# Performance work log

Measured on AMD Instinct MI355X. Metric: run time of the kernel, lower is better.

Reference implementation:

```python
import jax, jax.numpy as jnp
import numpy as np

N_NODES = 50000
N_EDGES = 800000
DIM = 64


def setup_inputs() -> dict:
    key = jax.random.key(0)
    ks = jax.random.split(key, 11)
    d = DIM
    node_embeddings = jax.random.normal(ks[0], (N_NODES, d), dtype=jnp.float32)
    neighbour_attributes = jax.random.normal(ks[1], (N_EDGES, d), dtype=jnp.float32)
    batch_index = jnp.sort(jax.random.randint(ks[2], (N_EDGES,), 0, N_NODES))
    s_align = 1.0 / np.sqrt(2 * d)
    s_d = 1.0 / np.sqrt(d)
    # alignment_layer: Linear(2d -> 1)
    align_w = jax.random.uniform(ks[3], (1, 2 * d), jnp.float32, -s_align, s_align)
    align_b = jax.random.uniform(ks[4], (1,), jnp.float32, -s_align, s_align)
    # context_layer: Linear(d -> d)
    ctx_w = jax.random.uniform(ks[5], (d, d), jnp.float32, -s_d, s_d)
    ctx_b = jax.random.uniform(ks[6], (d,), jnp.float32, -s_d, s_d)
    # readout_layer: GRUCell(d, d) -- torch layout [3d, d] gates (r, z, n)
    w_ih = jax.random.uniform(ks[7], (3 * d, d), jnp.float32, -s_d, s_d)
    w_hh = jax.random.uniform(ks[8], (3 * d, d), jnp.float32, -s_d, s_d)
    b_ih = jax.random.uniform(ks[9], (3 * d,), jnp.float32, -s_d, s_d)
    b_hh = jax.random.uniform(ks[10], (3 * d,), jnp.float32, -s_d, s_d)
    return {
        "node_embeddings": node_embeddings,
        "neighbour_attributes": neighbour_attributes,
        "batch_index": batch_index,
        "align_w": align_w, "align_b": align_b,
        "ctx_w": ctx_w, "ctx_b": ctx_b,
        "w_ih": w_ih, "w_hh": w_hh, "b_ih": b_ih, "b_hh": b_hh,
    }


def reference(node_embeddings, neighbour_attributes, batch_index,
              align_w, align_b, ctx_w, ctx_b, w_ih, w_hh, b_ih, b_hh):
    n = node_embeddings.shape[0]
    # _expand_and_join: gather node row per edge, concat with neighbour feats -> [E, 2d]
    joint = jnp.concatenate([node_embeddings[batch_index], neighbour_attributes], axis=1)
    # alignment + leaky_relu (torch default negative_slope=0.01); dropout is identity (p=0)
    scores = jax.nn.leaky_relu(joint @ align_w.T + align_b, negative_slope=0.01)[:, 0]  # [E]
    # segment softmax over variable-size neighbourhoods (torch_geometric softmax)
    seg_max = jax.ops.segment_max(scores, batch_index, num_segments=n)
    seg_max = jnp.where(jnp.isfinite(seg_max), seg_max, 0.0)  # guard empty segments
    ex = jnp.exp(scores - jax.lax.stop_gradient(seg_max)[batch_index])
    denom = jax.ops.segment_sum(ex, batch_index, num_segments=n)[batch_index]
    attn = (ex / jnp.maximum(denom, 1e-16))[:, None]  # [E, 1]
    # attention-weighted context messages, scatter-add pooled per node, then ELU
    msgs = attn * (neighbour_attributes @ ctx_w.T + ctx_b)  # [E, d]
    contexts = jax.nn.elu(jax.ops.segment_sum(msgs, batch_index, num_segments=n))  # [N, d]
    # GRUCell(contexts, node_embeddings), torch gate order (r, z, n)
    gi = contexts @ w_ih.T + b_ih
    gh = node_embeddings @ w_hh.T + b_hh
    i_r, i_z, i_n = jnp.split(gi, 3, axis=1)
    h_r, h_z, h_n = jnp.split(gh, 3, axis=1)
    r = jax.nn.sigmoid(i_r + h_r)
    z = jax.nn.sigmoid(i_z + h_z)
    g = jnp.tanh(i_n + r * h_n)
    h_new = (1.0 - z) * g + z * node_embeddings
    return jax.nn.relu(h_new)
```

## Files before the change

kernel.cpp:

```cpp
#include <hip/hip_runtime.h>
#include <stdint.h>

constexpr int kN = 50000;
constexpr int kE = 800000;
constexpr int kD = 64;

typedef short sv8 __attribute__((ext_vector_type(8)));
typedef float fv4 __attribute__((ext_vector_type(4)));

__device__ __forceinline__ float bf2f(uint16_t u) {
    union { uint32_t i; float f; } v; v.i = ((uint32_t)u) << 16; return v.f;
}
__device__ __forceinline__ uint16_t f2bf(float f) {
    union { float ff; uint32_t i; } v; v.ff = f;
    return (uint16_t)((v.i + 0x7FFFu + ((v.i >> 16) & 1u)) >> 16);
}
__device__ __forceinline__ float wsum64(float x) {
    x += __shfl_xor(x, 1);  x += __shfl_xor(x, 2);  x += __shfl_xor(x, 4);
    x += __shfl_xor(x, 8);  x += __shfl_xor(x, 16); x += __shfl_xor(x, 32);
    return x;
}

template<int BF> __device__ __forceinline__ float ldf(const void* p, int i) {
    if (BF) return bf2f(((const uint16_t*)p)[i]);
    return ((const float*)p)[i];
}
template<int BF> __device__ __forceinline__ void stf(void* p, int i, float v) {
    if (BF) ((uint16_t*)p)[i] = f2bf(v);
    else    ((float*)p)[i] = v;
}
template<int BF> __device__ __forceinline__ sv8 ldfrag(const void* p, int elem_base) {
    if (BF) {
        return *(const sv8*)((const uint16_t*)p + elem_base);
    } else {
        const float* f = (const float*)p + elem_base;
        sv8 r;
#pragma unroll
        for (int i = 0; i < 8; ++i) r[i] = (short)f2bf(f[i]);
        return r;
    }
}
__device__ __forceinline__ fv4 mfma16(sv8 a, sv8 b, fv4 c) {
    return __builtin_amdgcn_mfma_f32_16x16x32_bf16(a, b, c, 0, 0, 0);
}
template<int BF> __device__ __forceinline__ void ldrow(
    const void* nbr, int e, int t, float& v0, float& v1, float& v2, float& v3)
{
    if (BF) {
        uint2 u = *(const uint2*)((const uint16_t*)nbr + (size_t)e * kD + t * 4);
        v0 = bf2f((uint16_t)u.x); v1 = bf2f((uint16_t)(u.x >> 16));
        v2 = bf2f((uint16_t)u.y); v3 = bf2f((uint16_t)(u.y >> 16));
    } else {
        float4 f = *(const float4*)((const float*)nbr + (size_t)e * kD + t * 4);
        v0 = f.x; v1 = f.y; v2 = f.z; v3 = f.w;
    }
}

__global__ void k_prep(const int* __restrict__ bi, int* __restrict__ rp,
                       const uint16_t* __restrict__ nbr, int* __restrict__ flag) {
    if (blockIdx.x == gridDim.x - 1) {
        int lane = threadIdx.x;
        if (lane < 64) {
            float an = 0.f;
            for (int i = lane; i < 512; i += 64) {
                uint16_t u = nbr[i];
                if ((u & 0x7fffu) != 0) {
                    float a = fabsf(bf2f(u));
                    if (!(a >= 1e-8f && a <= 1e8f)) an += 1.f;
                }
            }
            an = wsum64(an);
            if (lane == 0) flag[0] = (an > 0.5f) ? 0 : 1;
        }
        return;
    }
    int n = blockIdx.x * 256 + threadIdx.x;
    if (n > kN) return;
    int lo = 0, hi = kE;
    int gl = n * 16 - 2048, gh = n * 16 + 2048;
    if (gl > 0 && gl < kE && bi[gl] < n)  lo = gl;
    if (gh > 0 && gh < kE && bi[gh] >= n) hi = gh;
    while (lo < hi) { int mid = (lo + hi) >> 1; if (bi[mid] < n) lo = mid + 1; else hi = mid; }
    rp[n] = lo;
}

template<int BF>
__device__ __forceinline__ void edges_body(
    const void* node_emb, const void* nbr, const void* align_w, const void* align_b,
    const int* __restrict__ rp, uint16_t* weighted, float* fhas)
{
    const int lane = threadIdx.x & 63;
    const int n    = blockIdx.x * 4 + (threadIdx.x >> 6);
    const int g    = lane >> 4;
    const int t    = lane & 15;

    float nd = wsum64(ldf<BF>(node_emb, n * kD + lane) * ldf<BF>(align_w, lane))
             + ldf<BF>(align_b, 0);

    float w0 = ldf<BF>(align_w, kD + t * 4 + 0);
    float w1 = ldf<BF>(align_w, kD + t * 4 + 1);
    float w2 = ldf<BF>(align_w, kD + t * 4 + 2);
    float w3 = ldf<BF>(align_w, kD + t * 4 + 3);

    const int s0 = rp[n], s1 = rp[n + 1];
    float l = 0.f, a0 = 0.f, a1 = 0.f, a2 = 0.f, a3 = 0.f;

    float c00, c01, c02, c03, c10, c11, c12, c13;
    {
        int e0 = s0 + g, e1 = s0 + g + 4;
        ldrow<BF>(nbr, (e0 < s1) ? e0 : 0, t, c00, c01, c02, c03);
        ldrow<BF>(nbr, (e1 < s1) ? e1 : 0, t, c10, c11, c12, c13);
    }

    for (int eb = s0; eb < s1; eb += 8) {
        float n00, n01, n02, n03, n10, n11, n12, n13;
        {
            int f0 = eb + 8 + g, f1 = eb + 12 + g;
            ldrow<BF>(nbr, (f0 < s1) ? f0 : 0, t, n00, n01, n02, n03);
            ldrow<BF>(nbr, (f1 < s1) ? f1 : 0, t, n10, n11, n12, n13);
        }
        float pa = c00 * w0 + c01 * w1 + c02 * w2 + c03 * w3;
        float pb = c10 * w0 + c11 * w1 + c12 * w2 + c13 * w3;
        pa += __shfl_xor(pa, 1);  pb += __shfl_xor(pb, 1);
        pa += __shfl_xor(pa, 2);  pb += __shfl_xor(pb, 2);
        pa += __shfl_xor(pa, 4);  pb += __shfl_xor(pb, 4);
        pa += __shfl_xor(pa, 8);  pb += __shfl_xor(pb, 8);
        float sa = pa + nd;  sa = (sa > 0.f) ? sa : 0.01f * sa;
        float sb = pb + nd;  sb = (sb > 0.f) ? sb : 0.01f * sb;
        float ea = (eb + g     < s1) ? __expf(sa) : 0.f;
        float eb2 = (eb + g + 4 < s1) ? __expf(sb) : 0.f;
        l  += ea + eb2;
        a0 += ea * c00 + eb2 * c10;
        a1 += ea * c01 + eb2 * c11;
        a2 += ea * c02 + eb2 * c12;
        a3 += ea * c03 + eb2 * c13;
        c00 = n00; c01 = n01; c02 = n02; c03 = n03;
        c10 = n10; c11 = n11; c12 = n12; c13 = n13;
    }

    l  += __shfl_xor(l, 16);   l  += __shfl_xor(l, 32);
    a0 += __shfl_xor(a0, 16);  a0 += __shfl_xor(a0, 32);
    a1 += __shfl_xor(a1, 16);  a1 += __shfl_xor(a1, 32);
    a2 += __shfl_xor(a2, 16);  a2 += __shfl_xor(a2, 32);
    a3 += __shfl_xor(a3, 16);  a3 += __shfl_xor(a3, 32);

    if (g == 0) {
        float inv = (s1 > s0) ? (1.f / l) : 0.f;
        uint32_t lo = (uint32_t)f2bf(a0 * inv) | ((uint32_t)f2bf(a1 * inv) << 16);
        uint32_t hi = (uint32_t)f2bf(a2 * inv) | ((uint32_t)f2bf(a3 * inv) << 16);
        *(uint2*)(weighted + (size_t)n * kD + t * 4) = make_uint2(lo, hi);
        if (t == 0) fhas[n] = (s1 > s0) ? 1.f : 0.f;
    }
}
__global__ __launch_bounds__(256, 4) void k_edges(
    const void* node_emb, const void* nbr, const void* aw, const void* ab,
    const int* __restrict__ rp, const int* __restrict__ flag,
    uint16_t* __restrict__ weighted, float* __restrict__ fhas)
{
    if (*flag) edges_body<1>(node_emb, nbr, aw, ab, rp, weighted, fhas);
    else       edges_body<0>(node_emb, nbr, aw, ab, rp, weighted, fhas);
}

template<int BF>
__device__ __forceinline__ void gru_body(
    const void* node_emb,
    const void* ctx_w, const void* ctx_b,
    const void* w_ih,  const void* w_hh,
    const void* b_ih,  const void* b_hh,
    const uint16_t* weighted, const float* fhas, void* out,
    uint16_t* swt,
    uint16_t (*sctx)[16][72])
{
    const int tid  = threadIdx.x;
    const int lane = tid & 63;
    const int wv   = tid >> 6;
    const int R    = blockIdx.x * 64 + wv * 16;
    const int t    = lane & 15;
    const int q    = lane >> 4;

    const fv4 zf = {0.f, 0.f, 0.f, 0.f};

    {
        const void* srcs[2] = { w_ih, w_hh };
#pragma unroll
        for (int hlf = 0; hlf < 2; ++hlf) {
            const void* src = srcs[hlf];
            uint16_t* dst = swt + hlf * 192 * 72;
            for (int off = tid * 8; off < 192 * 64; off += 256 * 8) {
                int r = off >> 6, c = off & 63;
                if (BF) {
                    *(uint4*)(dst + r * 72 + c) =
                        *(const uint4*)((const uint16_t*)src + off);
                } else {
                    const float* f = (const float*)src + off;
                    uint32_t p0 = (uint32_t)f2bf(f[0]) | ((uint32_t)f2bf(f[1]) << 16);
                    uint32_t p1 = (uint32_t)f2bf(f[2]) | ((uint32_t)f2bf(f[3]) << 16);
                    uint32_t p2 = (uint32_t)f2bf(f[4]) | ((uint32_t)f2bf(f[5]) << 16);
                    uint32_t p3 = (uint32_t)f2bf(f[6]) | ((uint32_t)f2bf(f[7]) << 16);
                    *(uint4*)(dst + r * 72 + c) = make_uint4(p0, p1, p2, p3);
                }
            }
        }
    }

    int ar = R + t; if (ar > kN - 1) ar = kN - 1;
    sv8 ah0 = ldfrag<BF>(node_emb, ar * kD + q * 8);
    sv8 ah1 = ldfrag<BF>(node_emb, ar * kD + q * 8 + 32);
    sv8 aw0 = ldfrag<1>(weighted, ar * kD + q * 8);
    sv8 aw1 = ldfrag<1>(weighted, ar * kD + q * 8 + 32);

    __syncthreads();

    fv4 accC[4];
#pragma unroll
    for (int ct = 0; ct < 4; ++ct) {
        int rb = (ct * 16 + t) * kD + q * 8;
        fv4 a = zf;
        a = mfma16(aw0, ldfrag<BF>(ctx_w, rb),      a);
        a = mfma16(aw1, ldfrag<BF>(ctx_w, rb + 32), a);
        accC[ct] = a;
    }

    float has_i[4];
#pragma unroll
    for (int i = 0; i < 4; ++i) {
        int node = R + q * 4 + i; if (node > kN - 1) node = kN - 1;
        has_i[i] = fhas[node];
    }
#pragma unroll
    for (int ct = 0; ct < 4; ++ct) {
        int col = ct * 16 + t;
        float cb = ldf<BF>(ctx_b, col);
#pragma unroll
        for (int i = 0; i < 4; ++i) {
            float x = accC[ct][i] + has_i[i] * cb;
            x = (x > 0.f) ? x : (__expf(x) - 1.f);
            sctx[wv][q * 4 + i][col] = f2bf(x);
        }
    }
    __syncthreads();

    sv8 ac0 = *(const sv8*)&sctx[wv][t][q * 8];
    sv8 ac1 = *(const sv8*)&sctx[wv][t][q * 8 + 32];

    const uint16_t* ih = swt;
    const uint16_t* hh = swt + 192 * 72;

#pragma unroll
    for (int jt = 0; jt < 4; ++jt) {
        const int rr = jt * 16 + t;
        fv4 air = zf, aiz = zf, ain = zf, ahr = zf, ahz = zf, ahn = zf;
        air = mfma16(ac0, *(const sv8*)&ih[ rr        * 72 + q * 8],      air);
        air = mfma16(ac1, *(const sv8*)&ih[ rr        * 72 + q * 8 + 32], air);
        aiz = mfma16(ac0, *(const sv8*)&ih[(rr +  64) * 72 + q * 8],      aiz);
        aiz = mfma16(ac1, *(const sv8*)&ih[(rr +  64) * 72 + q * 8 + 32], aiz);
        ain = mfma16(ac0, *(const sv8*)&ih[(rr + 128) * 72 + q * 8],      ain);
        ain = mfma16(ac1, *(const sv8*)&ih[(rr + 128) * 72 + q * 8 + 32], ain);
        ahr = mfma16(ah0, *(const sv8*)&hh[ rr        * 72 + q * 8],      ahr);
        ahr = mfma16(ah1, *(const sv8*)&hh[ rr        * 72 + q * 8 + 32], ahr);
        ahz = mfma16(ah0, *(const sv8*)&hh[(rr +  64) * 72 + q * 8],      ahz);
        ahz = mfma16(ah1, *(const sv8*)&hh[(rr +  64) * 72 + q * 8 + 32], ahz);
        ahn = mfma16(ah0, *(const sv8*)&hh[(rr + 128) * 72 + q * 8],      ahn);
        ahn = mfma16(ah1, *(const sv8*)&hh[(rr + 128) * 72 + q * 8 + 32], ahn);

        const int col = jt * 16 + t;
        float bir = ldf<BF>(b_ih, col),       bhr = ldf<BF>(b_hh, col);
        float biz = ldf<BF>(b_ih, 64 + col),  bhz = ldf<BF>(b_hh, 64 + col);
        float bin = ldf<BF>(b_ih, 128 + col), bhn = ldf<BF>(b_hh, 128 + col);
#pragma unroll
        for (int i = 0; i < 4; ++i) {
            int node = R + q * 4 + i;
            bool valid = node < kN;
            int cn = valid ? node : kN - 1;
            float hv = ldf<BF>(node_emb, cn * kD + col);
            float r = 1.f / (1.f + __expf(-(air[i] + bir + ahr[i] + bhr)));
            float z = 1.f / (1.f + __expf(-(aiz[i] + biz + ahz[i] + bhz)));
            float tt = ain[i] + bin + r * (ahn[i] + bhn);
            float gg = 2.f / (1.f + __expf(-2.f * tt)) - 1.f;
            float hn = (1.f - z) * gg + z * hv;
            if (valid) stf<BF>(out, node * kD + col, fmaxf(hn, 0.f));
        }
    }
}
__global__ __launch_bounds__(256, 2) void k_gru(
    const void* node_emb, const void* ctx_w, const void* ctx_b,
    const void* w_ih, const void* w_hh, const void* b_ih, const void* b_hh,
    const uint16_t* __restrict__ weighted, const float* __restrict__ fhas,
    const int* __restrict__ flag, void* out)
{
    __shared__ uint16_t swt[384 * 72];
    __shared__ uint16_t sctx[4][16][72];
    if (*flag) gru_body<1>(node_emb, ctx_w, ctx_b, w_ih, w_hh, b_ih, b_hh, weighted, fhas, out, swt, sctx);
    else       gru_body<0>(node_emb, ctx_w, ctx_b, w_ih, w_hh, b_ih, b_hh, weighted, fhas, out, swt, sctx);
}

extern "C" void kernel_launch(void* const* d_in, const int* in_sizes, int n_in,
                              void* d_out, int out_size, void* d_ws, size_t ws_size,
                              hipStream_t stream) {
    (void)in_sizes; (void)n_in; (void)out_size; (void)ws_size;
    const void* node_emb = d_in[0];
    const void* nbr      = d_in[1];
    const int*  bi       = (const int*)d_in[2];
    const void* align_w  = d_in[3];
    const void* align_b  = d_in[4];
    const void* ctx_w    = d_in[5];
    const void* ctx_b    = d_in[6];
    const void* w_ih     = d_in[7];
    const void* w_hh     = d_in[8];
    const void* b_ih     = d_in[9];
    const void* b_hh     = d_in[10];

    char* ws = (char*)d_ws;
    int*      row_ptr  = (int*)ws;
    int*      flag     = (int*)(ws + 200064);
    float*    fhas     = (float*)(ws + 204800);
    uint16_t* weighted = (uint16_t*)(ws + 409600);

    k_prep<<<(kN + 256) / 256 + 1, 256, 0, stream>>>(bi, row_ptr, (const uint16_t*)nbr, flag);
    k_edges<<<kN / 4, 256, 0, stream>>>(node_emb, nbr, align_w, align_b, row_ptr, flag, weighted, fhas);
    k_gru<<<(kN + 63) / 64, 256, 0, stream>>>(node_emb, ctx_w, ctx_b, w_ih, w_hh, b_ih, b_hh,
                                              weighted, fhas, flag, d_out);
}
```

Measured before the change: 345.1 us.

## Pre-convert GRU weights to bf16 in prep kernel and deepen edge prefetch

The prep kernel now converts ctx_w, w_ih and w_hh to bf16 once into workspace, and each prep block re-runs the dtype detection itself. The GRU kernel reads its MFMA weight fragments straight from global or L2 instead of staging 55KB into shared memory per block, which drops two __syncthreads and raises the occupancy bound from 2 to 4. The edge kernel processes 16 edges per iteration with a deeper prefetch, which costs more registers. The risk is extra global or L2 traffic for the weight fragments in the GRU kernel.

```diff
diff --git a/kernel.cpp b/kernel.cpp
--- a/kernel.cpp
+++ b/kernel.cpp
@@ -56,32 +56,63 @@
     }
 }
 
+__device__ __forceinline__ int detect_bf16(const uint16_t* __restrict__ nbr) {
+    const int lane = threadIdx.x & 63;
+    uint4 v = ((const uint4*)nbr)[lane];
+    uint32_t w[4] = { v.x, v.y, v.z, v.w };
+    float an = 0.f;
+#pragma unroll
+    for (int k = 0; k < 4; ++k) {
+#pragma unroll
+        for (int h = 0; h < 2; ++h) {
+            uint16_t u = (uint16_t)(w[k] >> (16 * h));
+            if ((u & 0x7fffu) != 0) {
+                float a = fabsf(bf2f(u));
+                if (!(a >= 1e-8f && a <= 1e8f)) an += 1.f;
+            }
+        }
+    }
+    an = wsum64(an);
+    return (an > 0.5f) ? 0 : 1;
+}
+
 __global__ void k_prep(const int* __restrict__ bi, int* __restrict__ rp,
-                       const uint16_t* __restrict__ nbr, int* __restrict__ flag) {
-    if (blockIdx.x == gridDim.x - 1) {
-        int lane = threadIdx.x;
-        if (lane < 64) {
-            float an = 0.f;
-            for (int i = lane; i < 512; i += 64) {
-                uint16_t u = nbr[i];
-                if ((u & 0x7fffu) != 0) {
-                    float a = fabsf(bf2f(u));
-                    if (!(a >= 1e-8f && a <= 1e8f)) an += 1.f;
-                }
-            }
-            an = wsum64(an);
-            if (lane == 0) flag[0] = (an > 0.5f) ? 0 : 1;
-        }
-        return;
-    }
-    int n = blockIdx.x * 256 + threadIdx.x;
-    if (n > kN) return;
-    int lo = 0, hi = kE;
-    int gl = n * 16 - 2048, gh = n * 16 + 2048;
-    if (gl > 0 && gl < kE && bi[gl] < n)  lo = gl;
-    if (gh > 0 && gh < kE && bi[gh] >= n) hi = gh;
-    while (lo < hi) { int mid = (lo + hi) >> 1; if (bi[mid] < n) lo = mid + 1; else hi = mid; }
-    rp[n] = lo;
+                       const uint16_t* __restrict__ nbr, int* __restrict__ flag,
+                       const void* __restrict__ ctx_w, const void* __restrict__ w_ih,
+                       const void* __restrict__ w_hh,
+                       uint16_t* __restrict__ cwbf, uint16_t* __restrict__ ihbf,
+                       uint16_t* __restrict__ hhbf) {
+    const int b = blockIdx.x;
+    if (b < 196) {
+        int n = b * 256 + threadIdx.x;
+        if (n > kN) return;
+        int lo = 0, hi = kE;
+        int gl = n * 16 - 2048, gh = n * 16 + 2048;
+        if (gl > 0 && gl < kE && bi[gl] < n)  lo = gl;
+        if (gh > 0 && gh < kE && bi[gh] >= n) hi = gh;
+        while (lo < hi) { int mid = (lo + hi) >> 1; if (bi[mid] < n) lo = mid + 1; else hi = mid; }
+        rp[n] = lo;
+    } else if (b == 196) {
+        if (threadIdx.x < 64) {
+            int bf = detect_bf16(nbr);
+            if (threadIdx.x == 0) flag[0] = bf;
+        }
+    } else {
+        const int base = (b - 197) * 1024 + threadIdx.x * 4;
+        const void* src; uint16_t* dst; int off;
+        if (base < 4096)       { src = ctx_w; dst = cwbf; off = base; }
+        else if (base < 16384) { src = w_ih;  dst = ihbf; off = base - 4096; }
+        else                   { src = w_hh;  dst = hhbf; off = base - 16384; }
+        const int bf = detect_bf16(nbr);
+        if (bf) {
+            *(uint2*)(dst + off) = *(const uint2*)((const uint16_t*)src + off);
+        } else {
+            float4 f = *(const float4*)((const float*)src + off);
+            uint32_t p0 = (uint32_t)f2bf(f.x) | ((uint32_t)f2bf(f.y) << 16);
+            uint32_t p1 = (uint32_t)f2bf(f.z) | ((uint32_t)f2bf(f.w) << 16);
+            *(uint2*)(dst + off) = make_uint2(p0, p1);
+        }
+    }
 }
 
 template<int BF>
@@ -106,36 +137,54 @@
     float l = 0.f, a0 = 0.f, a1 = 0.f, a2 = 0.f, a3 = 0.f;
 
     float c00, c01, c02, c03, c10, c11, c12, c13;
+    float c20, c21, c22, c23, c30, c31, c32, c33;
     {
-        int e0 = s0 + g, e1 = s0 + g + 4;
+        int e0 = s0 + g, e1 = s0 + g + 4, e2 = s0 + g + 8, e3 = s0 + g + 12;
         ldrow<BF>(nbr, (e0 < s1) ? e0 : 0, t, c00, c01, c02, c03);
         ldrow<BF>(nbr, (e1 < s1) ? e1 : 0, t, c10, c11, c12, c13);
-    }
-
-    for (int eb = s0; eb < s1; eb += 8) {
-        float n00, n01, n02, n03, n10, n11, n12, n13;
+        ldrow<BF>(nbr, (e2 < s1) ? e2 : 0, t, c20, c21, c22, c23);
+        ldrow<BF>(nbr, (e3 < s1) ? e3 : 0, t, c30, c31, c32, c33);
+    }
+
+    for (int eb = s0; eb < s1; eb += 16) {
+        float m00, m01, m02, m03, m10, m11, m12, m13;
+        float m20, m21, m22, m23, m30, m31, m32, m33;
         {
-            int f0 = eb + 8 + g, f1 = eb + 12 + g;
-            ldrow<BF>(nbr, (f0 < s1) ? f0 : 0, t, n00, n01, n02, n03);
-            ldrow<BF>(nbr, (f1 < s1) ? f1 : 0, t, n10, n11, n12, n13);
-        }
-        float pa = c00 * w0 + c01 * w1 + c02 * w2 + c03 * w3;
-        float pb = c10 * w0 + c11 * w1 + c12 * w2 + c13 * w3;
-        pa += __shfl_xor(pa, 1);  pb += __shfl_xor(pb, 1);
-        pa += __shfl_xor(pa, 2);  pb += __shfl_xor(pb, 2);
-        pa += __shfl_xor(pa, 4);  pb += __shfl_xor(pb, 4);
-        pa += __shfl_xor(pa, 8);  pb += __shfl_xor(pb, 8);
-        float sa = pa + nd;  sa = (sa > 0.f) ? sa : 0.01f * sa;
-        float sb = pb + nd;  sb = (sb > 0.f) ? sb : 0.01f * sb;
-        float ea = (eb + g     < s1) ? __expf(sa) : 0.f;
-        float eb2 = (eb + g + 4 < s1) ? __expf(sb) : 0.f;
-        l  += ea + eb2;
-        a0 += ea * c00 + eb2 * c10;
-        a1 += ea * c01 + eb2 * c11;
-        a2 += ea * c02 + eb2 * c12;
-        a3 += ea * c03 + eb2 * c13;
-        c00 = n00; c01 = n01; c02 = n02; c03 = n03;
-        c10 = n10; c11 = n11; c12 = n12; c13 = n13;
+            int f0 = eb + 16 + g, f1 = eb + 20 + g, f2 = eb + 24 + g, f3 = eb + 28 + g;
+            ldrow<BF>(nbr, (f0 < s1) ? f0 : 0, t, m00, m01, m02, m03);
+            ldrow<BF>(nbr, (f1 < s1) ? f1 : 0, t, m10, m11, m12, m13);
+            ldrow<BF>(nbr, (f2 < s1) ? f2 : 0, t, m20, m21, m22, m23);
+            ldrow<BF>(nbr, (f3 < s1) ? f3 : 0, t, m30, m31, m32, m33);
+        }
+        float p0 = c00 * w0 + c01 * w1 + c02 * w2 + c03 * w3;
+        float p1 = c10 * w0 + c11 * w1 + c12 * w2 + c13 * w3;
+        float p2 = c20 * w0 + c21 * w1 + c22 * w2 + c23 * w3;
+        float p3 = c30 * w0 + c31 * w1 + c32 * w2 + c33 * w3;
+        p0 += __shfl_xor(p0, 1); p1 += __shfl_xor(p1, 1);
+        p2 += __shfl_xor(p2, 1); p3 += __shfl_xor(p3, 1);
+        p0 += __shfl_xor(p0, 2); p1 += __shfl_xor(p1, 2);
+        p2 += __shfl_xor(p2, 2); p3 += __shfl_xor(p3, 2);
+        p0 += __shfl_xor(p0, 4); p1 += __shfl_xor(p1, 4);
+        p2 += __shfl_xor(p2, 4); p3 += __shfl_xor(p3, 4);
+        p0 += __shfl_xor(p0, 8); p1 += __shfl_xor(p1, 8);
+        p2 += __shfl_xor(p2, 8); p3 += __shfl_xor(p3, 8);
+        float s0f = p0 + nd;  s0f = (s0f > 0.f) ? s0f : 0.01f * s0f;
+        float s1f = p1 + nd;  s1f = (s1f > 0.f) ? s1f : 0.01f * s1f;
+        float s2f = p2 + nd;  s2f = (s2f > 0.f) ? s2f : 0.01f * s2f;
+        float s3f = p3 + nd;  s3f = (s3f > 0.f) ? s3f : 0.01f * s3f;
+        float e0 = (eb + g      < s1) ? __expf(s0f) : 0.f;
+        float e1 = (eb + g + 4  < s1) ? __expf(s1f) : 0.f;
+        float e2 = (eb + g + 8  < s1) ? __expf(s2f) : 0.f;
+        float e3 = (eb + g + 12 < s1) ? __expf(s3f) : 0.f;
+        l  += (e0 + e1) + (e2 + e3);
+        a0 += e0 * c00 + e1 * c10 + e2 * c20 + e3 * c30;
+        a1 += e0 * c01 + e1 * c11 + e2 * c21 + e3 * c31;
+        a2 += e0 * c02 + e1 * c12 + e2 * c22 + e3 * c32;
+        a3 += e0 * c03 + e1 * c13 + e2 * c23 + e3 * c33;
+        c00 = m00; c01 = m01; c02 = m02; c03 = m03;
+        c10 = m10; c11 = m11; c12 = m12; c13 = m13;
+        c20 = m20; c21 = m21; c22 = m22; c23 = m23;
+        c30 = m30; c31 = m31; c32 = m32; c33 = m33;
     }
 
     l  += __shfl_xor(l, 16);   l  += __shfl_xor(l, 32);
@@ -163,45 +212,20 @@
 
 template<int BF>
 __device__ __forceinline__ void gru_body(
-    const void* node_emb,
-    const void* ctx_w, const void* ctx_b,
-    const void* w_ih,  const void* w_hh,
+    const void* node_emb, const void* ctx_b,
     const void* b_ih,  const void* b_hh,
+    const uint16_t* __restrict__ cwbf, const uint16_t* __restrict__ ihbf,
+    const uint16_t* __restrict__ hhbf,
     const uint16_t* weighted, const float* fhas, void* out,
-    uint16_t* swt,
     uint16_t (*sctx)[16][72])
 {
-    const int tid  = threadIdx.x;
-    const int lane = tid & 63;
-    const int wv   = tid >> 6;
+    const int lane = threadIdx.x & 63;
+    const int wv   = threadIdx.x >> 6;
     const int R    = blockIdx.x * 64 + wv * 16;
     const int t    = lane & 15;
     const int q    = lane >> 4;
 
     const fv4 zf = {0.f, 0.f, 0.f, 0.f};
-
-    {
-        const void* srcs[2] = { w_ih, w_hh };
-#pragma unroll
-        for (int hlf = 0; hlf < 2; ++hlf) {
-            const void* src = srcs[hlf];
-            uint16_t* dst = swt + hlf * 192 * 72;
-            for (int off = tid * 8; off < 192 * 64; off += 256 * 8) {
-                int r = off >> 6, c = off & 63;
-                if (BF) {
-                    *(uint4*)(dst + r * 72 + c) =
-                        *(const uint4*)((const uint16_t*)src + off);
-                } else {
-                    const float* f = (const float*)src + off;
-                    uint32_t p0 = (uint32_t)f2bf(f[0]) | ((uint32_t)f2bf(f[1]) << 16);
-                    uint32_t p1 = (uint32_t)f2bf(f[2]) | ((uint32_t)f2bf(f[3]) << 16);
-                    uint32_t p2 = (uint32_t)f2bf(f[4]) | ((uint32_t)f2bf(f[5]) << 16);
-                    uint32_t p3 = (uint32_t)f2bf(f[6]) | ((uint32_t)f2bf(f[7]) << 16);
-                    *(uint4*)(dst + r * 72 + c) = make_uint4(p0, p1, p2, p3);
-                }
-            }
-        }
-    }
 
     int ar = R + t; if (ar > kN - 1) ar = kN - 1;
     sv8 ah0 = ldfrag<BF>(node_emb, ar * kD + q * 8);
@@ -209,15 +233,13 @@
     sv8 aw0 = ldfrag<1>(weighted, ar * kD + q * 8);
     sv8 aw1 = ldfrag<1>(weighted, ar * kD + q * 8 + 32);
 
-    __syncthreads();
-
     fv4 accC[4];
 #pragma unroll
     for (int ct = 0; ct < 4; ++ct) {
         int rb = (ct * 16 + t) * kD + q * 8;
         fv4 a = zf;
-        a = mfma16(aw0, ldfrag<BF>(ctx_w, rb),      a);
-        a = mfma16(aw1, ldfrag<BF>(ctx_w, rb + 32), a);
+        a = mfma16(aw0, *(const sv8*)&cwbf[rb],      a);
+        a = mfma16(aw1, *(const sv8*)&cwbf[rb + 32], a);
         accC[ct] = a;
     }
 
@@ -238,30 +260,26 @@
             sctx[wv][q * 4 + i][col] = f2bf(x);
         }
     }
-    __syncthreads();
 
     sv8 ac0 = *(const sv8*)&sctx[wv][t][q * 8];
     sv8 ac1 = *(const sv8*)&sctx[wv][t][q * 8 + 32];
 
-    const uint16_t* ih = swt;
-    const uint16_t* hh = swt + 192 * 72;
-
 #pragma unroll
     for (int jt = 0; jt < 4; ++jt) {
-        const int rr = jt * 16 + t;
+        const int rr = (jt * 16 + t) * kD + q * 8;
         fv4 air = zf, aiz = zf, ain = zf, ahr = zf, ahz = zf, ahn = zf;
-        air = mfma16(ac0, *(const sv8*)&ih[ rr        * 72 + q * 8],      air);
-        air = mfma16(ac1, *(const sv8*)&ih[ rr        * 72 + q * 8 + 32], air);
-        aiz = mfma16(ac0, *(const sv8*)&ih[(rr +  64) * 72 + q * 8],      aiz);
-        aiz = mfma16(ac1, *(const sv8*)&ih[(rr +  64) * 72 + q * 8 + 32], aiz);
-        ain = mfma16(ac0, *(const sv8*)&ih[(rr + 128) * 72 + q * 8],      ain);
-        ain = mfma16(ac1, *(const sv8*)&ih[(rr + 128) * 72 + q * 8 + 32], ain);
-        ahr = mfma16(ah0, *(const sv8*)&hh[ rr        * 72 + q * 8],      ahr);
-        ahr = mfma16(ah1, *(const sv8*)&hh[ rr        * 72 + q * 8 + 32], ahr);
-        ahz = mfma16(ah0, *(const sv8*)&hh[(rr +  64) * 72 + q * 8],      ahz);
-        ahz = mfma16(ah1, *(const sv8*)&hh[(rr +  64) * 72 + q * 8 + 32], ahz);
-        ahn = mfma16(ah0, *(const sv8*)&hh[(rr + 128) * 72 + q * 8],      ahn);
-        ahn = mfma16(ah1, *(const sv8*)&hh[(rr + 128) * 72 + q * 8 + 32], ahn);
+        air = mfma16(ac0, *(const sv8*)&ihbf[rr],             air);
+        air = mfma16(ac1, *(const sv8*)&ihbf[rr + 32],        air);
+        aiz = mfma16(ac0, *(const sv8*)&ihbf[rr + 64 * kD],      aiz);
+        aiz = mfma16(ac1, *(const sv8*)&ihbf[rr + 64 * kD + 32], aiz);
+        ain = mfma16(ac0, *(const sv8*)&ihbf[rr + 128 * kD],      ain);
+        ain = mfma16(ac1, *(const sv8*)&ihbf[rr + 128 * kD + 32], ain);
+        ahr = mfma16(ah0, *(const sv8*)&hhbf[rr],             ahr);
+        ahr = mfma16(ah1, *(const sv8*)&hhbf[rr + 32],        ahr);
+        ahz = mfma16(ah0, *(const sv8*)&hhbf[rr + 64 * kD],      ahz);
+        ahz = mfma16(ah1, *(const sv8*)&hhbf[rr + 64 * kD + 32], ahz);
+        ahn = mfma16(ah0, *(const sv8*)&hhbf[rr + 128 * kD],      ahn);
+        ahn = mfma16(ah1, *(const sv8*)&hhbf[rr + 128 * kD + 32], ahn);
 
         const int col = jt * 16 + t;
         float bir = ldf<BF>(b_ih, col),       bhr = ldf<BF>(b_hh, col);
@@ -282,16 +300,17 @@
         }
     }
 }
-__global__ __launch_bounds__(256, 2) void k_gru(
-    const void* node_emb, const void* ctx_w, const void* ctx_b,
-    const void* w_ih, const void* w_hh, const void* b_ih, const void* b_hh,
+__global__ __launch_bounds__(256, 4) void k_gru(
+    const void* node_emb, const void* ctx_b,
+    const void* b_ih, const void* b_hh,
+    const uint16_t* __restrict__ cwbf, const uint16_t* __restrict__ ihbf,
+    const uint16_t* __restrict__ hhbf,
     const uint16_t* __restrict__ weighted, const float* __restrict__ fhas,
     const int* __restrict__ flag, void* out)
 {
-    __shared__ uint16_t swt[384 * 72];
     __shared__ uint16_t sctx[4][16][72];
-    if (*flag) gru_body<1>(node_emb, ctx_w, ctx_b, w_ih, w_hh, b_ih, b_hh, weighted, fhas, out, swt, sctx);
-    else       gru_body<0>(node_emb, ctx_w, ctx_b, w_ih, w_hh, b_ih, b_hh, weighted, fhas, out, swt, sctx);
+    if (*flag) gru_body<1>(node_emb, ctx_b, b_ih, b_hh, cwbf, ihbf, hhbf, weighted, fhas, out, sctx);
+    else       gru_body<0>(node_emb, ctx_b, b_ih, b_hh, cwbf, ihbf, hhbf, weighted, fhas, out, sctx);
 }
 
 extern "C" void kernel_launch(void* const* d_in, const int* in_sizes, int n_in,
@@ -315,9 +334,13 @@
     int*      flag     = (int*)(ws + 200064);
     float*    fhas     = (float*)(ws + 204800);
     uint16_t* weighted = (uint16_t*)(ws + 409600);
-
-    k_prep<<<(kN + 256) / 256 + 1, 256, 0, stream>>>(bi, row_ptr, (const uint16_t*)nbr, flag);
+    uint16_t* cwbf     = (uint16_t*)(ws + 6809600);
+    uint16_t* ihbf     = (uint16_t*)(ws + 6817792);
+    uint16_t* hhbf     = (uint16_t*)(ws + 6842368);
+
+    k_prep<<<225, 256, 0, stream>>>(bi, row_ptr, (const uint16_t*)nbr, flag,
+                                    ctx_w, w_ih, w_hh, cwbf, ihbf, hhbf);
     k_edges<<<kN / 4, 256, 0, stream>>>(node_emb, nbr, align_w, align_b, row_ptr, flag, weighted, fhas);
-    k_gru<<<(kN + 63) / 64, 256, 0, stream>>>(node_emb, ctx_w, ctx_b, w_ih, w_hh, b_ih, b_hh,
-                                              weighted, fhas, flag, d_out);
-}
+    k_gru<<<(kN + 63) / 64, 256, 0, stream>>>(node_emb, ctx_b, b_ih, b_hh,
+                                              cwbf, ihbf, hhbf, weighted, fhas, flag, d_out);
+}
```

Result: no change. 344.0 us (-0.3%).
